# Optimization experiments

Measured on AMD Instinct MI355X. Metric: run time of the kernel, lower is better.

## Reference

```python
import jax, jax.numpy as jnp
import numpy as np

N_NODES = 50000
N_EDGES = 800000
D_IN = 256
D_HID = 256
D_OUT = 16
N_GRAPHS = 128
DROPOUT_P = 0.5


def setup_inputs() -> dict:
    key = jax.random.key(0)
    ks = jax.random.split(key, 8)
    x = jax.random.normal(ks[0], (N_NODES, D_IN), dtype=jnp.float32)
    edge_index = jax.random.randint(ks[1], (2, N_EDGES), 0, N_NODES, dtype=jnp.int64)
    edge_weight = jax.random.uniform(ks[2], (N_EDGES,), dtype=jnp.float32)
    index = jnp.sort(jax.random.randint(ks[3], (N_NODES,), 0, N_GRAPHS, dtype=jnp.int64))
    W1 = jax.random.normal(ks[4], (D_IN, D_HID), dtype=jnp.float32) / np.sqrt(D_IN)
    b1 = jnp.zeros((D_HID,), dtype=jnp.float32)
    fc_W = jax.random.normal(ks[5], (D_HID, D_OUT), dtype=jnp.float32) / np.sqrt(D_HID)
    fc_b = jnp.zeros((D_OUT,), dtype=jnp.float32)
    return {"x": x, "edge_index": edge_index, "edge_weight": edge_weight,
            "index": index, "W1": W1, "b1": b1, "fc_W": fc_W, "fc_b": fc_b}


def gcn_conv(x, edge_index, edge_weight, W, b):
    # PyG GCNConv: add self loops (weight 1), symmetric degree norm, linear-then-propagate.
    n = x.shape[0]
    loops = jnp.arange(n, dtype=edge_index.dtype)
    row = jnp.concatenate([edge_index[0], loops])   # source nodes
    col = jnp.concatenate([edge_index[1], loops])   # target nodes (aggregation)
    ew = jnp.concatenate([edge_weight, jnp.ones((n,), dtype=x.dtype)])
    deg = jax.ops.segment_sum(ew, col, num_segments=n)
    dinv = jnp.where(deg > 0, jax.lax.rsqrt(deg), 0.0)
    norm = dinv[row] * ew * dinv[col]               # [E+N]
    h = x @ W                                       # [N, hid]
    msg = norm[:, None] * h[row]                    # gather + scale
    out = jax.ops.segment_sum(msg, col, num_segments=n)  # scatter-add
    return out + b


def reference(x, edge_index, edge_weight, index, W1, b1, fc_W, fc_b):
    h = gcn_conv(x, edge_index, edge_weight, W1, b1)
    h = jax.nn.relu(h)
    # dropout (training mode, p=0.5) with a fixed key for determinism
    keep = jax.random.bernoulli(jax.random.key(42), 1.0 - DROPOUT_P, h.shape)
    h = jnp.where(keep, h / (1.0 - DROPOUT_P), 0.0)
    # global mean pool over graph ids
    sums = jax.ops.segment_sum(h, index, num_segments=N_GRAPHS)          # [G, hid]
    cnts = jax.ops.segment_sum(jnp.ones((h.shape[0],), h.dtype), index, num_segments=N_GRAPHS)
    pooled = sums / jnp.maximum(cnts, 1.0)[:, None]
    return pooled @ fc_W + fc_b
```

## Files before the change

kernel.cpp:

```cpp
#include <hip/hip_runtime.h>
#include <hip/hip_fp16.h>
#include <stdint.h>

#define N_NODES  50000
#define N_EDGES  800000
#define D        256
#define D_OUT    16
#define N_GRAPHS 128
#define NB_SCAN  196
#define FILL_NB  3125
#define BCAP     64


typedef short bf16x8 __attribute__((ext_vector_type(8)));
typedef float f32x4  __attribute__((ext_vector_type(4)));
typedef float f32x2  __attribute__((ext_vector_type(2)));

__device__ __forceinline__ uint32_t rotl32(uint32_t x, int d) {
    return (x << d) | (x >> (32 - d));
}

__device__ __forceinline__ void threefry2x32(uint32_t k0, uint32_t k1,
                                             uint32_t c0, uint32_t c1,
                                             uint32_t& o0, uint32_t& o1) {
    uint32_t ks2 = k0 ^ k1 ^ 0x1BD11BDAu;
    uint32_t x0 = c0 + k0, x1 = c1 + k1;
    x0 += x1; x1 = rotl32(x1, 13); x1 ^= x0;
    x0 += x1; x1 = rotl32(x1, 15); x1 ^= x0;
    x0 += x1; x1 = rotl32(x1, 26); x1 ^= x0;
    x0 += x1; x1 = rotl32(x1, 6);  x1 ^= x0;
    x0 += k1; x1 += ks2 + 1u;
    x0 += x1; x1 = rotl32(x1, 17); x1 ^= x0;
    x0 += x1; x1 = rotl32(x1, 29); x1 ^= x0;
    x0 += x1; x1 = rotl32(x1, 16); x1 ^= x0;
    x0 += x1; x1 = rotl32(x1, 24); x1 ^= x0;
    x0 += ks2; x1 += k0 + 2u;
    x0 += x1; x1 = rotl32(x1, 13); x1 ^= x0;
    x0 += x1; x1 = rotl32(x1, 15); x1 ^= x0;
    x0 += x1; x1 = rotl32(x1, 26); x1 ^= x0;
    x0 += x1; x1 = rotl32(x1, 6);  x1 ^= x0;
    x0 += k0; x1 += k1 + 3u;
    x0 += x1; x1 = rotl32(x1, 17); x1 ^= x0;
    x0 += x1; x1 = rotl32(x1, 29); x1 ^= x0;
    x0 += x1; x1 = rotl32(x1, 16); x1 ^= x0;
    x0 += x1; x1 = rotl32(x1, 24); x1 ^= x0;
    x0 += k1; x1 += ks2 + 4u;
    x0 += x1; x1 = rotl32(x1, 13); x1 ^= x0;
    x0 += x1; x1 = rotl32(x1, 15); x1 ^= x0;
    x0 += x1; x1 = rotl32(x1, 26); x1 ^= x0;
    x0 += x1; x1 = rotl32(x1, 6);  x1 ^= x0;
    x0 += ks2; x1 += k0 + 5u;
    o0 = x0; o1 = x1;
}

__device__ __forceinline__ bool dropout_keep(uint32_t i) {
    uint32_t o0, o1;
    threefry2x32(0u, 42u, 0u, i, o0, o1);
    return ((o0 ^ o1) & 0x80000000u) == 0u;
}

__device__ __forceinline__ uint32_t bf16_rne(float f) {
    uint32_t u = __float_as_uint(f);
    return (u + 0x7FFFu + ((u >> 16) & 1u)) >> 16;
}

__global__ __launch_bounds__(256) void k_build(const float* __restrict__ W,
                                               ushort* __restrict__ wt,
                                               const int* __restrict__ ei,
                                               const float* __restrict__ ew,
                                               double* __restrict__ degsum,
                                               int2* __restrict__ bucket) {
    int t = threadIdx.x;
    if (blockIdx.x < 16) {
        __shared__ float td[64][65];
        int kb = blockIdx.x & 3, nb = blockIdx.x >> 2;
        int nl = t & 63, r4 = t >> 6;
#pragma unroll
        for (int i = 0; i < 16; i++) {
            int kl = r4 + 4 * i;
            td[kl][nl] = W[(size_t)(kb * 64 + kl) * 256 + nb * 64 + nl];
        }
        __syncthreads();
        int kp = t & 31, nl2 = t >> 5;
        uint32_t* wt32 = (uint32_t*)wt;
#pragma unroll
        for (int i = 0; i < 8; i++) {
            int n = nl2 + 8 * i;
            uint32_t p = bf16_rne(td[2 * kp][n]) | (bf16_rne(td[2 * kp + 1][n]) << 16);
            wt32[((size_t)(nb * 64 + n) * 256 + kb * 64 + 2 * kp) >> 1] = p;
        }
    } else {
        int e = (blockIdx.x - 16) * 256 + t;
        int r = ei[e];
        int c = ei[N_EDGES + e];
        float w = ew[e];
        double old = atomicAdd(&degsum[c], 4294967296.0 + (double)w);
        int pos = (int)(old * (1.0 / 4294967296.0));
        bucket[(size_t)c * BCAP + pos] = make_int2(r * 32, __float_as_int(w));
    }
}

__global__ __launch_bounds__(256) void k_dinv(const double* __restrict__ degsum,
                                              float* __restrict__ dinv,
                                              int* __restrict__ cnt,
                                              float* __restrict__ sums) {
    int i = blockIdx.x * 256 + threadIdx.x;
    if (i < N_NODES) {
        double val = degsum[i];
        int c = (int)(val * (1.0 / 4294967296.0));
        float deg = (float)(val - (double)c * 4294967296.0) + 1.0f;
        dinv[i] = rsqrtf(deg);
        cnt[i] = c;
    }
    if (i < N_GRAPHS * D) sums[i] = 0.0f;
}

__device__ __forceinline__ int swz(int row, int kByte) {
    return (row << 9) + (kByte ^ ((row & 7) << 4));
}

__global__ __launch_bounds__(256) void k_gemm(const float* __restrict__ x,
                                              const ushort* __restrict__ wt,
                                              const float* __restrict__ dinv,
                                              uint8_t* __restrict__ hb) {
    __shared__ __align__(16) char smem[73728];
    __shared__ float sdinv[64];
    int tid = threadIdx.x;
    int Mbase = blockIdx.x * 64;

    if (tid < 64) {
        int node = Mbase + tid; if (node >= N_NODES) node = N_NODES - 1;
        sdinv[tid] = dinv[node];
    }
    const float4* xv = (const float4*)x;
#pragma unroll
    for (int i = 0; i < 16; i++) {
        int f = tid + i * 256;
        int r = f >> 6;
        int c4 = f & 63;
        int node = Mbase + r; if (node >= N_NODES) node = N_NODES - 1;
        float4 v = xv[(size_t)node * 64 + c4];
        uint32_t p0 = bf16_rne(v.x) | (bf16_rne(v.y) << 16);
        uint32_t p1 = bf16_rne(v.z) | (bf16_rne(v.w) << 16);
        *(uint2*)(smem + swz(r, c4 * 8)) = make_uint2(p0, p1);
    }

    int l = tid & 63;
    int w = tid >> 6;
    int wr = w >> 1, wc = w & 1;
    int lr = l & 15;
    int kg = l >> 4;
    int drow = (l >> 4) * 4;
    int dcol = l & 15;
    const uint4* wt4 = (const uint4*)wt;
    ushort* c_lds = (ushort*)(smem + 65536);

    for (int nb = 0; nb < 4; nb++) {
#pragma unroll
        for (int i = 0; i < 8; i++) {
            int f = tid + i * 256;
            int r = f >> 5;
            int c = f & 31;
            uint4 v = wt4[(size_t)(nb * 64 + r) * 32 + c];
            *(uint4*)(smem + 32768 + swz(r, c * 16)) = v;
        }
        __syncthreads();

        f32x4 acc00 = {0.f, 0.f, 0.f, 0.f};
        f32x4 acc01 = acc00, acc10 = acc00, acc11 = acc00;
#pragma unroll
        for (int ks = 0; ks < 8; ks++) {
            int kB = ks * 64 + kg * 16;
            bf16x8 a0 = *(const bf16x8*)(smem + swz(wr * 32 + lr, kB));
            bf16x8 a1 = *(const bf16x8*)(smem + swz(wr * 32 + 16 + lr, kB));
            bf16x8 b0 = *(const bf16x8*)(smem + 32768 + swz(wc * 32 + lr, kB));
            bf16x8 b1 = *(const bf16x8*)(smem + 32768 + swz(wc * 32 + 16 + lr, kB));
            acc00 = __builtin_amdgcn_mfma_f32_16x16x32_bf16(a0, b0, acc00, 0, 0, 0);
            acc01 = __builtin_amdgcn_mfma_f32_16x16x32_bf16(a0, b1, acc01, 0, 0, 0);
            acc10 = __builtin_amdgcn_mfma_f32_16x16x32_bf16(a1, b0, acc10, 0, 0, 0);
            acc11 = __builtin_amdgcn_mfma_f32_16x16x32_bf16(a1, b1, acc11, 0, 0, 0);
        }
#pragma unroll
        for (int r = 0; r < 4; r++) {
            int lr0 = wr * 32 + drow + r;
            float s0 = sdinv[lr0], s1 = sdinv[lr0 + 16];
            int cc = wc * 32 + dcol;
            __half h00 = __float2half(acc00[r] * s0);
            __half h01 = __float2half(acc01[r] * s0);
            __half h10 = __float2half(acc10[r] * s1);
            __half h11 = __float2half(acc11[r] * s1);
            c_lds[lr0 * 64 + cc]             = *(ushort*)&h00;
            c_lds[lr0 * 64 + cc + 16]        = *(ushort*)&h01;
            c_lds[(lr0 + 16) * 64 + cc]      = *(ushort*)&h10;
            c_lds[(lr0 + 16) * 64 + cc + 16] = *(ushort*)&h11;
        }
        __syncthreads();
#pragma unroll
        for (int i = 0; i < 2; i++) {
            int idx = tid + i * 256;
            int r = idx >> 3;
            int c8 = idx & 7;
            uint4 v = ((const uint4*)c_lds)[idx];
            __half2* hp = (__half2*)&v;
            float f0 = __low2float(hp[0]), f1 = __high2float(hp[0]);
            float f2 = __low2float(hp[1]), f3 = __high2float(hp[1]);
            float f4 = __low2float(hp[2]), f5 = __high2float(hp[2]);
            float f6 = __low2float(hp[3]), f7 = __high2float(hp[3]);
            uint32_t w0 = __builtin_amdgcn_cvt_pk_fp8_f32(f0, f1, 0, false);
            w0 = __builtin_amdgcn_cvt_pk_fp8_f32(f2, f3, w0, true);
            uint32_t w1 = __builtin_amdgcn_cvt_pk_fp8_f32(f4, f5, 0, false);
            w1 = __builtin_amdgcn_cvt_pk_fp8_f32(f6, f7, w1, true);
            int node = Mbase + r;
            if (node < N_NODES)
                *(uint2*)(hb + (size_t)node * 256 + nb * 64 + c8 * 8) =
                    make_uint2(w0, w1);
        }
    }
}

__device__ __forceinline__ void fma8f(float* a, uint2 u, float w) {
    f32x2 p0 = __builtin_amdgcn_cvt_pk_f32_fp8(u.x, false);
    f32x2 p1 = __builtin_amdgcn_cvt_pk_f32_fp8(u.x, true);
    f32x2 p2 = __builtin_amdgcn_cvt_pk_f32_fp8(u.y, false);
    f32x2 p3 = __builtin_amdgcn_cvt_pk_f32_fp8(u.y, true);
    a[0] = fmaf(w, p0.x, a[0]); a[1] = fmaf(w, p0.y, a[1]);
    a[2] = fmaf(w, p1.x, a[2]); a[3] = fmaf(w, p1.y, a[3]);
    a[4] = fmaf(w, p2.x, a[4]); a[5] = fmaf(w, p2.y, a[5]);
    a[6] = fmaf(w, p3.x, a[6]); a[7] = fmaf(w, p3.y, a[7]);
}

__global__ __launch_bounds__(256) void k_agg(const int* __restrict__ cnt,
                                             const int2* __restrict__ bucket,
                                             const uint8_t* __restrict__ hb,
                                             const float* __restrict__ dinv,
                                             const float* __restrict__ b1,
                                             const int* __restrict__ gidx,
                                             float* __restrict__ sums) {
    __shared__ float ls[4][256];
    int wid = threadIdx.x >> 6;
    int l = threadIdx.x & 63;
    int half = l >> 5;
    int cl = l & 31;
    int n = blockIdx.x * 4 + wid;
    const uint2* h8 = (const uint2*)hb;
    int cn = cnt[n];
    int s = n * BCAP;
    int e = s + cn;
    int last = e - 1;

    uint2 un = h8[(size_t)n * 32 + cl];
    float4 bv = ((const float4*)b1)[2 * cl + half];
    float dn = dinv[n];
    int gfirst = gidx[blockIdx.x * 4];
    int glast  = gidx[blockIdx.x * 4 + 3];

    int off = 4 * half;
    int col = 8 * cl + off;

    int j = s;
    int2 E0, E1, E2, E3;
    if (j < e) {
        int i0 = j + half;
        E0 = bucket[i0];
        E1 = bucket[i0 + 2];
        E2 = bucket[i0 + 4];
        E3 = bucket[i0 + 6];
    }

    uint32_t base = (uint32_t)n * D + (uint32_t)col;
    float m0 = dropout_keep(base + 0u) ? 2.f : 0.f;
    float m1 = dropout_keep(base + 1u) ? 2.f : 0.f;
    float m2 = dropout_keep(base + 2u) ? 2.f : 0.f;
    float m3 = dropout_keep(base + 3u) ? 2.f : 0.f;

    float A0[8] = {0,0,0,0,0,0,0,0}, A1[8] = {0,0,0,0,0,0,0,0};

    for (; j + 8 <= e; j += 8) {
        uint2 u0 = h8[(size_t)(uint32_t)(E0.x + cl)];
        uint2 u1 = h8[(size_t)(uint32_t)(E1.x + cl)];
        uint2 u2 = h8[(size_t)(uint32_t)(E2.x + cl)];
        uint2 u3 = h8[(size_t)(uint32_t)(E3.x + cl)];
        float w0 = __int_as_float(E0.y);
        float w1 = __int_as_float(E1.y);
        float w2 = __int_as_float(E2.y);
        float w3 = __int_as_float(E3.y);
        int i0n = j + 8 + half;
        E0 = bucket[i0n];
        E1 = bucket[i0n + 2];
        E2 = bucket[i0n + 4];
        E3 = bucket[i0n + 6];
        fma8f(A0, u0, w0); fma8f(A1, u1, w1);
        fma8f(A0, u2, w2); fma8f(A1, u3, w3);
    }
    if (j < e) {
        int x0 = j + half, x1 = x0 + 2, x2 = x0 + 4, x3 = x0 + 6;
        int c0 = x0 < last ? x0 : last;
        int c1 = x1 < last ? x1 : last;
        int c2 = x2 < last ? x2 : last;
        int c3 = x3 < last ? x3 : last;
        int2 F0 = bucket[c0], F1 = bucket[c1], F2 = bucket[c2], F3 = bucket[c3];
        uint2 u0 = h8[(size_t)(uint32_t)(F0.x + cl)];
        uint2 u1 = h8[(size_t)(uint32_t)(F1.x + cl)];
        uint2 u2 = h8[(size_t)(uint32_t)(F2.x + cl)];
        uint2 u3 = h8[(size_t)(uint32_t)(F3.x + cl)];
        float w0 = x0 <= last ? __int_as_float(F0.y) : 0.f;
        float w1 = x1 <= last ? __int_as_float(F1.y) : 0.f;
        float w2 = x2 <= last ? __int_as_float(F2.y) : 0.f;
        float w3 = x3 <= last ? __int_as_float(F3.y) : 0.f;
        fma8f(A0, u0, w0); fma8f(A1, u1, w1);
        fma8f(A0, u2, w2); fma8f(A1, u3, w3);
    }

    float full[8];
#pragma unroll
    for (int k = 0; k < 8; k++)
        full[k] = A0[k] + A1[k];
#pragma unroll
    for (int k = 0; k < 8; k++)
        full[k] += __shfl_xor(full[k], 32, 64);

    uint32_t word = half ? un.y : un.x;
    f32x2 q0 = __builtin_amdgcn_cvt_pk_f32_fp8(word, false);
    f32x2 q1 = __builtin_amdgcn_cvt_pk_f32_fp8(word, true);
    float v0 = fmaxf(dn * (full[off + 0] + q0.x) + bv.x, 0.f) * m0;
    float v1 = fmaxf(dn * (full[off + 1] + q0.y) + bv.y, 0.f) * m1;
    float v2 = fmaxf(dn * (full[off + 2] + q1.x) + bv.z, 0.f) * m2;
    float v3 = fmaxf(dn * (full[off + 3] + q1.y) + bv.w, 0.f) * m3;

    if (gfirst == glast) {
        *(float4*)&ls[wid][col] = make_float4(v0, v1, v2, v3);
        __syncthreads();
        int t = threadIdx.x;
        float sv = (ls[0][t] + ls[1][t]) + (ls[2][t] + ls[3][t]);
        atomicAdd(&sums[(size_t)gfirst * D + t], sv);
    } else {
        int g = gidx[n];
        float* sg = &sums[(size_t)g * D + col];
        atomicAdd(sg + 0, v0);
        atomicAdd(sg + 1, v1);
        atomicAdd(sg + 2, v2);
        atomicAdd(sg + 3, v3);
    }
}

__global__ __launch_bounds__(256) void k_out(const float* __restrict__ sums,
                                             const int* __restrict__ gidx,
                                             const float* __restrict__ fcW,
                                             const float* __restrict__ fcb,
                                             float* __restrict__ out) {
    __shared__ int sh[2];
    __shared__ float p[D];
    int g = blockIdx.x, t = threadIdx.x;
    if (t == 0) {
        int lo = 0, hi = N_NODES;
        while (lo < hi) { int m = (lo + hi) >> 1; if (gidx[m] < g) lo = m + 1; else hi = m; }
        sh[0] = lo;
        int lo2 = lo; hi = N_NODES;
        while (lo2 < hi) { int m = (lo2 + hi) >> 1; if (gidx[m] < g + 1) lo2 = m + 1; else hi = m; }
        sh[1] = lo2;
    }
    __syncthreads();
    float c = fmaxf((float)(sh[1] - sh[0]), 1.0f);
    p[t] = sums[(size_t)g * D + t] / c;
    __syncthreads();
    if (t < D_OUT) {
        float acc = fcb[t];
        for (int k = 0; k < D; k++)
            acc = fmaf(p[k], fcW[k * D_OUT + t], acc);
        out[g * D_OUT + t] = acc;
    }
}

extern "C" void kernel_launch(void* const* d_in, const int* in_sizes, int n_in,
                              void* d_out, int out_size, void* d_ws, size_t ws_size,
                              hipStream_t stream) {
    const float* x   = (const float*)d_in[0];
    const int*   ei  = (const int*)d_in[1];
    const float* ew  = (const float*)d_in[2];
    const int*   gix = (const int*)d_in[3];
    const float* W1  = (const float*)d_in[4];
    const float* b1  = (const float*)d_in[5];
    const float* fcW = (const float*)d_in[6];
    const float* fcb = (const float*)d_in[7];
    float* out = (float*)d_out;

    float*   ws     = (float*)d_ws;
    float*   dinv   = ws;
    uint8_t* hb     = (uint8_t*)(ws + 65536);
    int2*    bucket = (int2*)(ws + 65536 + 3200000);
    int*     cnt    = (int*)(bucket + (size_t)N_NODES * BCAP);
    ushort*  wt     = (ushort*)(cnt + 65536);
    float*   sums   = (float*)(wt + 65536);
    double*  degsum = (double*)(sums + 32768);

    hipMemsetAsync(degsum, 0, N_NODES * sizeof(double), stream);

    k_build<<<16 + FILL_NB, 256, 0, stream>>>(W1, wt, ei, ew, degsum, bucket);
    k_dinv<<<NB_SCAN, 256, 0, stream>>>(degsum, dinv, cnt, sums);
    k_gemm<<<(N_NODES + 63) / 64, 256, 0, stream>>>(x, wt, dinv, hb);
    k_agg<<<N_NODES / 4, 256, 0, stream>>>(cnt, bucket, hb, dinv, b1, gix, sums);
    k_out<<<N_GRAPHS, 256, 0, stream>>>(sums, gix, fcW, fcb, out);
}
```

Before: 157.8 us.

## Pack edge buckets to 32-bit records, fold dinv kernel into GEMM

```diff
diff --git a/kernel.cpp b/kernel.cpp
--- a/kernel.cpp
+++ b/kernel.cpp
@@ -7,7 +7,6 @@
 #define D        256
 #define D_OUT    16
 #define N_GRAPHS 128
-#define NB_SCAN  196
 #define FILL_NB  3125
 #define BCAP     64
 
@@ -64,12 +63,18 @@
     return (u + 0x7FFFu + ((u >> 16) & 1u)) >> 16;
 }
 
+__device__ __forceinline__ uint32_t cvt_pk_bf16(float lo, float hi) {
+    uint32_t r;
+    asm("v_cvt_pk_bf16_f32 %0, %1, %2" : "=v"(r) : "v"(lo), "v"(hi));
+    return r;
+}
+
 __global__ __launch_bounds__(256) void k_build(const float* __restrict__ W,
                                                ushort* __restrict__ wt,
                                                const int* __restrict__ ei,
                                                const float* __restrict__ ew,
                                                double* __restrict__ degsum,
-                                               int2* __restrict__ bucket) {
+                                               uint32_t* __restrict__ bucket) {
     int t = threadIdx.x;
     if (blockIdx.x < 16) {
         __shared__ float td[64][65];
@@ -96,41 +101,42 @@
         float w = ew[e];
         double old = atomicAdd(&degsum[c], 4294967296.0 + (double)w);
         int pos = (int)(old * (1.0 / 4294967296.0));
-        bucket[(size_t)c * BCAP + pos] = make_int2(r * 32, __float_as_int(w));
-    }
-}
-
-__global__ __launch_bounds__(256) void k_dinv(const double* __restrict__ degsum,
+        __half hw = __float2half(w);
+        bucket[(size_t)c * BCAP + pos] =
+            ((uint32_t)r << 16) | (uint32_t)__half_as_ushort(hw);
+    }
+}
+
+__device__ __forceinline__ int swz(int row, int kByte) {
+    return (row << 9) + (kByte ^ ((row & 7) << 4));
+}
+
+__global__ __launch_bounds__(256) void k_gemm(const float* __restrict__ x,
+                                              const ushort* __restrict__ wt,
+                                              const double* __restrict__ degsum,
                                               float* __restrict__ dinv,
                                               int* __restrict__ cnt,
-                                              float* __restrict__ sums) {
-    int i = blockIdx.x * 256 + threadIdx.x;
-    if (i < N_NODES) {
-        double val = degsum[i];
-        int c = (int)(val * (1.0 / 4294967296.0));
-        float deg = (float)(val - (double)c * 4294967296.0) + 1.0f;
-        dinv[i] = rsqrtf(deg);
-        cnt[i] = c;
-    }
-    if (i < N_GRAPHS * D) sums[i] = 0.0f;
-}
-
-__device__ __forceinline__ int swz(int row, int kByte) {
-    return (row << 9) + (kByte ^ ((row & 7) << 4));
-}
-
-__global__ __launch_bounds__(256) void k_gemm(const float* __restrict__ x,
-                                              const ushort* __restrict__ wt,
-                                              const float* __restrict__ dinv,
+                                              float* __restrict__ sums,
                                               uint8_t* __restrict__ hb) {
     __shared__ __align__(16) char smem[73728];
     __shared__ float sdinv[64];
     int tid = threadIdx.x;
     int Mbase = blockIdx.x * 64;
 
+    if (blockIdx.x < 128) sums[blockIdx.x * 256 + tid] = 0.0f;
     if (tid < 64) {
-        int node = Mbase + tid; if (node >= N_NODES) node = N_NODES - 1;
-        sdinv[tid] = dinv[node];
+        int node = Mbase + tid;
+        if (node < N_NODES) {
+            double val = degsum[node];
+            int c = (int)(val * (1.0 / 4294967296.0));
+            float deg = (float)(val - (double)c * 4294967296.0) + 1.0f;
+            float di = rsqrtf(deg);
+            sdinv[tid] = di;
+            dinv[node] = di;
+            cnt[node] = c;
+        } else {
+            sdinv[tid] = 0.0f;
+        }
     }
     const float4* xv = (const float4*)x;
 #pragma unroll
@@ -140,8 +146,8 @@
         int c4 = f & 63;
         int node = Mbase + r; if (node >= N_NODES) node = N_NODES - 1;
         float4 v = xv[(size_t)node * 64 + c4];
-        uint32_t p0 = bf16_rne(v.x) | (bf16_rne(v.y) << 16);
-        uint32_t p1 = bf16_rne(v.z) | (bf16_rne(v.w) << 16);
+        uint32_t p0 = cvt_pk_bf16(v.x, v.y);
+        uint32_t p1 = cvt_pk_bf16(v.z, v.w);
         *(uint2*)(smem + swz(r, c4 * 8)) = make_uint2(p0, p1);
     }
 
@@ -229,8 +235,13 @@
     a[6] = fmaf(w, p3.x, a[6]); a[7] = fmaf(w, p3.y, a[7]);
 }
 
+__device__ __forceinline__ float rec_w(uint32_t rec) {
+    __half h = __ushort_as_half((ushort)(rec & 0xFFFFu));
+    return __half2float(h);
+}
+
 __global__ __launch_bounds__(256) void k_agg(const int* __restrict__ cnt,
-                                             const int2* __restrict__ bucket,
+                                             const uint32_t* __restrict__ bucket,
                                              const uint8_t* __restrict__ hb,
                                              const float* __restrict__ dinv,
                                              const float* __restrict__ b1,
@@ -258,7 +269,7 @@
     int col = 8 * cl + off;
 
     int j = s;
-    int2 E0, E1, E2, E3;
+    uint32_t E0, E1, E2, E3;
     if (j < e) {
         int i0 = j + half;
         E0 = bucket[i0];
@@ -276,14 +287,14 @@
     float A0[8] = {0,0,0,0,0,0,0,0}, A1[8] = {0,0,0,0,0,0,0,0};
 
     for (; j + 8 <= e; j += 8) {
-        uint2 u0 = h8[(size_t)(uint32_t)(E0.x + cl)];
-        uint2 u1 = h8[(size_t)(uint32_t)(E1.x + cl)];
-        uint2 u2 = h8[(size_t)(uint32_t)(E2.x + cl)];
-        uint2 u3 = h8[(size_t)(uint32_t)(E3.x + cl)];
-        float w0 = __int_as_float(E0.y);
-        float w1 = __int_as_float(E1.y);
-        float w2 = __int_as_float(E2.y);
-        float w3 = __int_as_float(E3.y);
+        uint2 u0 = h8[(size_t)(uint32_t)(((E0 >> 16) << 5) + cl)];
+        uint2 u1 = h8[(size_t)(uint32_t)(((E1 >> 16) << 5) + cl)];
+        uint2 u2 = h8[(size_t)(uint32_t)(((E2 >> 16) << 5) + cl)];
+        uint2 u3 = h8[(size_t)(uint32_t)(((E3 >> 16) << 5) + cl)];
+        float w0 = rec_w(E0);
+        float w1 = rec_w(E1);
+        float w2 = rec_w(E2);
+        float w3 = rec_w(E3);
         int i0n = j + 8 + half;
         E0 = bucket[i0n];
         E1 = bucket[i0n + 2];
@@ -298,15 +309,16 @@
         int c1 = x1 < last ? x1 : last;
         int c2 = x2 < last ? x2 : last;
         int c3 = x3 < last ? x3 : last;
-        int2 F0 = bucket[c0], F1 = bucket[c1], F2 = bucket[c2], F3 = bucket[c3];
-        uint2 u0 = h8[(size_t)(uint32_t)(F0.x + cl)];
-        uint2 u1 = h8[(size_t)(uint32_t)(F1.x + cl)];
-        uint2 u2 = h8[(size_t)(uint32_t)(F2.x + cl)];
-        uint2 u3 = h8[(size_t)(uint32_t)(F3.x + cl)];
-        float w0 = x0 <= last ? __int_as_float(F0.y) : 0.f;
-        float w1 = x1 <= last ? __int_as_float(F1.y) : 0.f;
-        float w2 = x2 <= last ? __int_as_float(F2.y) : 0.f;
-        float w3 = x3 <= last ? __int_as_float(F3.y) : 0.f;
+        uint32_t F0 = bucket[c0], F1 = bucket[c1];
+        uint32_t F2 = bucket[c2], F3 = bucket[c3];
+        uint2 u0 = h8[(size_t)(uint32_t)(((F0 >> 16) << 5) + cl)];
+        uint2 u1 = h8[(size_t)(uint32_t)(((F1 >> 16) << 5) + cl)];
+        uint2 u2 = h8[(size_t)(uint32_t)(((F2 >> 16) << 5) + cl)];
+        uint2 u3 = h8[(size_t)(uint32_t)(((F3 >> 16) << 5) + cl)];
+        float w0 = x0 <= last ? rec_w(F0) : 0.f;
+        float w1 = x1 <= last ? rec_w(F1) : 0.f;
+        float w2 = x2 <= last ? rec_w(F2) : 0.f;
+        float w3 = x3 <= last ? rec_w(F3) : 0.f;
         fma8f(A0, u0, w0); fma8f(A1, u1, w1);
         fma8f(A0, u2, w2); fma8f(A1, u3, w3);
     }
@@ -384,20 +396,19 @@
     const float* fcb = (const float*)d_in[7];
     float* out = (float*)d_out;
 
-    float*   ws     = (float*)d_ws;
-    float*   dinv   = ws;
-    uint8_t* hb     = (uint8_t*)(ws + 65536);
-    int2*    bucket = (int2*)(ws + 65536 + 3200000);
-    int*     cnt    = (int*)(bucket + (size_t)N_NODES * BCAP);
-    ushort*  wt     = (ushort*)(cnt + 65536);
-    float*   sums   = (float*)(wt + 65536);
-    double*  degsum = (double*)(sums + 32768);
+    float*    ws     = (float*)d_ws;
+    float*    dinv   = ws;
+    uint8_t*  hb     = (uint8_t*)(ws + 65536);
+    uint32_t* bucket = (uint32_t*)(ws + 65536 + 3200000);
+    int*      cnt    = (int*)(bucket + (size_t)N_NODES * BCAP + 16);
+    ushort*   wt     = (ushort*)(cnt + 65536);
+    float*    sums   = (float*)(wt + 65536);
+    double*   degsum = (double*)(sums + 32768);
 
     hipMemsetAsync(degsum, 0, N_NODES * sizeof(double), stream);
 
     k_build<<<16 + FILL_NB, 256, 0, stream>>>(W1, wt, ei, ew, degsum, bucket);
-    k_dinv<<<NB_SCAN, 256, 0, stream>>>(degsum, dinv, cnt, sums);
-    k_gemm<<<(N_NODES + 63) / 64, 256, 0, stream>>>(x, wt, dinv, hb);
+    k_gemm<<<(N_NODES + 63) / 64, 256, 0, stream>>>(x, wt, degsum, dinv, cnt, sums, hb);
     k_agg<<<N_NODES / 4, 256, 0, stream>>>(cnt, bucket, hb, dinv, b1, gix, sums);
     k_out<<<N_GRAPHS, 256, 0, stream>>>(sums, gix, fcW, fcb, out);
 }
```

Measured after the change: 156.5 us. No clear change (-0.8%).
